# Kernel tuning notes

Measured on AMD Instinct MI355X. Metric: run time of the kernel, lower is better.

Reference implementation:

```python
import jax, jax.numpy as jnp
from jax import lax
import numpy as np

EPS = 1e-7  # keras.backend.epsilon()
DISCOUNT = 1.0

B, T, S, F = 32, 128, 64, 256  # samples, sentences, steps, features


def setup_inputs() -> dict:
    key = jax.random.key(0)
    ks = jax.random.split(key, 6)
    scale = 1.0 / np.sqrt(F)
    return {
        "x": jax.random.normal(ks[0], (B, T, S, F), dtype=jnp.float32),
        "W": jax.random.normal(ks[1], (F, F), dtype=jnp.float32) * scale,
        "W_context": jax.random.normal(ks[2], (F, F), dtype=jnp.float32) * scale,
        "W_l": jax.random.normal(ks[3], (F,), dtype=jnp.float32) * scale,
        "W_lc": jax.random.normal(ks[4], (F,), dtype=jnp.float32) * scale,
        "bl": jnp.zeros((1,), dtype=jnp.float32),
        "b": jnp.zeros((F,), dtype=jnp.float32),
        "u": jax.random.normal(ks[5], (F,), dtype=jnp.float32) * scale,
    }


def _forward(x, W, W_context, W_l, W_lc, bl, b, u):
    # x: [B, T, S, F]; scan over sentence axis T with carried context [B, F].
    def step(carry, x_):
        context, count = carry            # context: [B, F]
        context_ = context                # aggregate == 'sum'
        uit = jnp.einsum("bsf,fg->bsg", x_, W)            # [B, S, F]
        c = context_ @ W_context                            # [B, F]
        # gate: l = sigmoid(<context, W_lc> + bl broadcast over steps + <x, W_l>)
        gate_logit = (context_ @ W_lc + bl[0])[:, None] + x_ @ W_l  # [B, S]
        l = jax.nn.sigmoid(gate_logit)[..., None]           # [B, S, 1]
        uit = jnp.tanh(l * uit + (1.0 - l) * c[:, None, :] + b)
        ait = uit @ u                                        # [B, S]
        a = jnp.exp(ait)
        a = a / (jnp.sum(a, axis=1, keepdims=True) + EPS)   # masked-softmax (no mask)
        attended = jnp.einsum("bsf,bs->bf", x_, a)          # [B, F]
        new_context = context * DISCOUNT + attended
        return (new_context, count + 1.0), (attended, a, new_context)

    x_t = jnp.transpose(x, (1, 0, 2, 3))  # [T, B, S, F]
    init = (jnp.zeros((x.shape[0], x.shape[-1]), x.dtype), jnp.asarray(0.0, x.dtype))
    _, (out, weights, ctx) = lax.scan(step, init, x_t)
    output = jnp.transpose(out, (1, 0, 2))       # [B, T, F]
    context = jnp.transpose(ctx, (1, 0, 2))      # [B, T, F]
    weights = jnp.transpose(weights, (1, 0, 2))  # [B, T, S]
    return output, context, weights


def reference(x, W, W_context, W_l, W_lc, bl, b, u):
    return _forward(x, W, W_context, W_l, W_lc, bl, b, u)
```

## Files before the change

kernel.cpp:

```cpp
#include <hip/hip_runtime.h>
#include <stdint.h>

#define Tdim 128
#define Bdim 32
#define Sdim 64
#define Fdim 256

typedef unsigned short u16;
typedef short bf16x8 __attribute__((ext_vector_type(8)));
typedef float f32x4 __attribute__((ext_vector_type(4)));

#define K2     2.8853900817779268f
#define LOG2E  1.4426950408889634f

__device__ __forceinline__ u16 f2b(float f){
  union { float f; uint32_t u; } v; v.f = f;
  uint32_t u = v.u;
  if ((u & 0x7fffffffu) > 0x7f800000u) return (u16)0x7fc0;
  uint32_t r = (u + 0x7fffu + ((u >> 16) & 1u)) >> 16;
  return (u16)r;
}
__device__ __forceinline__ float b2f(u16 h){
  union { uint32_t u; float f; } v; v.u = ((uint32_t)h) << 16; return v.f;
}
__device__ __forceinline__ float b2f_lo(uint32_t w){
  union { uint32_t u; float f; } v; v.u = w << 16; return v.f;
}
__device__ __forceinline__ float b2f_hi(uint32_t w){
  union { uint32_t u; float f; } v; v.u = w & 0xffff0000u; return v.f;
}
__device__ __forceinline__ uint32_t pack2(float a, float b){
  return (uint32_t)f2b(a) | ((uint32_t)f2b(b) << 16);
}
__device__ __forceinline__ uint4 pack8(const float4 a, const float4 b){
  uint4 r;
  r.x = pack2(a.x, a.y); r.y = pack2(a.z, a.w);
  r.z = pack2(b.x, b.y); r.w = pack2(b.z, b.w);
  return r;
}

__device__ __forceinline__ void bar_lds(){
  asm volatile("s_waitcnt lgkmcnt(0)" ::: "memory");
  __builtin_amdgcn_s_barrier();
  asm volatile("" ::: "memory");
}


__global__ __launch_bounds__(256) void kt_transpose_cvt(const float* __restrict__ Wg,
                                                        u16* __restrict__ Wt){
  __shared__ u16 tile[64*66];
  int bx = blockIdx.x;
  int ti = bx >> 2, tj = bx & 3;
  int t = threadIdx.x;
#pragma unroll
  for (int i = 0; i < 16; ++i){
    int e = t*16 + i;
    int r = e >> 6, c = e & 63;
    tile[r*66 + c] = f2b(Wg[(ti*64 + r)*256 + tj*64 + c]);
  }
  __syncthreads();
#pragma unroll
  for (int i = 0; i < 16; ++i){
    int e = t*16 + i;
    int r = e >> 6, c = e & 63;
    Wt[(tj*64 + r)*256 + ti*64 + c] = tile[c*66 + r];
  }
}

__global__ __launch_bounds__(512, 4) void kt_gemm2(const float* __restrict__ Xg,
                                                   const u16* __restrict__ Wt,
                                                   const float* __restrict__ Wlg,
                                                   u16* __restrict__ Pg,
                                                   float* __restrict__ qg){
  __shared__ u16 Ws[256*72];
  __shared__ u16 Xs[128*72];
  __shared__ float Wls[256];
  int t  = threadIdx.x;
  int r0 = blockIdx.x * 128;
  if (t < 256) Wls[t] = Wlg[t];
  int lane = t & 63, wv = t >> 6;
  int goff = (wv & 3)*64, roff = (wv >> 2)*64;
  int fr = lane & 15, fq = lane >> 4;
  f32x4 acc[4][4];
#pragma unroll
  for (int a = 0; a < 4; ++a)
#pragma unroll
    for (int b = 0; b < 4; ++b)
      acc[a][b] = (f32x4){0.f,0.f,0.f,0.f};
  float qacc = 0.f;

  for (int kk = 0; kk < 4; ++kk){
    int k0 = kk*64;
    __syncthreads();
#pragma unroll
    for (int uu = 0; uu < 4; ++uu){
      int unit = uu*512 + t;
      int row = unit >> 3, c = unit & 7;
      *(uint4*)&Ws[row*72 + c*8] = *(const uint4*)&Wt[row*256 + k0 + c*8];
    }
#pragma unroll
    for (int uu = 0; uu < 2; ++uu){
      int unit = uu*512 + t;
      int row = unit >> 3, c = unit & 7;
      const float4* xp = (const float4*)&Xg[(size_t)(r0+row)*256 + k0 + c*8];
      *(uint4*)&Xs[row*72 + c*8] = pack8(xp[0], xp[1]);
    }
    __syncthreads();
    if (t < 128){
      int r = t;
#pragma unroll
      for (int c = 0; c < 8; ++c){
        uint4 xv = *(const uint4*)&Xs[r*72 + c*8];
        const uint32_t* xw = (const uint32_t*)&xv;
#pragma unroll
        for (int p = 0; p < 4; ++p){
          qacc = fmaf(b2f_lo(xw[p]), Wls[k0 + c*8 + 2*p],     qacc);
          qacc = fmaf(b2f_hi(xw[p]), Wls[k0 + c*8 + 2*p + 1], qacc);
        }
      }
    }
#pragma unroll
    for (int ks = 0; ks < 64; ks += 32){
      bf16x8 af[4], bf_[4];
#pragma unroll
      for (int mi = 0; mi < 4; ++mi)
        af[mi] = *(const bf16x8*)&Ws[(goff + mi*16 + fr)*72 + ks + fq*8];
#pragma unroll
      for (int ni = 0; ni < 4; ++ni)
        bf_[ni] = *(const bf16x8*)&Xs[(roff + ni*16 + fr)*72 + ks + fq*8];
#pragma unroll
      for (int mi = 0; mi < 4; ++mi)
#pragma unroll
        for (int ni = 0; ni < 4; ++ni)
          acc[mi][ni] = __builtin_amdgcn_mfma_f32_16x16x32_bf16(
              af[mi], bf_[ni], acc[mi][ni], 0, 0, 0);
    }
  }
#pragma unroll
  for (int mi = 0; mi < 4; ++mi){
    int g = goff + mi*16 + fq*4;
    int grp = g >> 4;
#pragma unroll
    for (int ni = 0; ni < 4; ++ni){
      int r = r0 + roff + ni*16 + fr;
      int bt = r >> 6, s = r & 63;
      ushort4 st;
      st.x = f2b(acc[mi][ni][0]); st.y = f2b(acc[mi][ni][1]);
      st.z = f2b(acc[mi][ni][2]); st.w = f2b(acc[mi][ni][3]);
      *(ushort4*)&Pg[(size_t)bt*16384 + grp*1024 + s*16 + fq*4] = st;
    }
  }
  if (t < 128) qg[r0 + t] = qacc;
}

__global__ __launch_bounds__(1024, 4) void kt_scan6(
    const float* __restrict__ Xg, const u16* __restrict__ Pf,
    const float* __restrict__ qf, const float* __restrict__ Wcg,
    const float* __restrict__ Wlcg, const float* __restrict__ blg,
    const float* __restrict__ biasg, const float* __restrict__ ug,
    float* __restrict__ out)
{
  __shared__ float ctx_s[256], bbr_s[256], ur_s[256], wlc_s[256];
  __shared__ float pp[64*17];
  __shared__ float attp[16*260];
  __shared__ float glc_p[4];

  const int tid   = threadIdx.x;
  const int b     = blockIdx.x;
  const int lane  = tid & 63;
  const int wave  = tid >> 6;
  const int g_loc = lane >> 2;
  const int fc    = lane & 3;
  const int gcol  = wave*16 + g_loc;
  const int f     = tid & 255;

  uint32_t wcp2[32];
#pragma unroll
  for (int i = 0; i < 16; ++i){
    int m  = (4*fc + i) & 15;
    int fb = fc*64 + m*4;
    wcp2[2*i]   = pack2(Wcg[(fb+0)*256 + gcol], Wcg[(fb+1)*256 + gcol]);
    wcp2[2*i+1] = pack2(Wcg[(fb+2)*256 + gcol], Wcg[(fb+3)*256 + gcol]);
  }

  if (tid < 256){
    ctx_s[tid] = 0.f;
    bbr_s[tid] = K2 * biasg[tid];
    ur_s[tid]  = ug[tid];
    wlc_s[tid] = Wlcg[tid];
  }
  if (tid < 4) glc_p[tid] = 0.f;
  const float blf = blg[0];
  float glcr = 0.f;

  const u16*    pP = Pf + (size_t)(b*Tdim)*16384 + wave*1024 + lane*16;
  const float4* pX = (const float4*)Xg + (size_t)(b*Tdim)*4096 + wave*256 + lane;
  const float*  pq = qf + (size_t)(b*Tdim)*64 + lane;

  uint32_t pw[8];
  {
    const uint4* pp_ = (const uint4*)pP;
    *(uint4*)&pw[0] = pp_[0]; *(uint4*)&pw[4] = pp_[1];
  }
  float qcur = pq[0];

  float* outO = out;
  float* outC = out + Bdim*Tdim*Fdim;
  float* outW = out + 2*Bdim*Tdim*Fdim;
  __syncthreads();

  for (int tt = 0; tt < Tdim; ++tt){
    const int bt    = b*Tdim + tt;
    const int nstep = (tt < Tdim-1) ? 1 : 0;

    uint32_t pwn[8];
    {
      const uint4* pp_ = (const uint4*)(pP + (size_t)nstep*16384);
      *(uint4*)&pwn[0] = pp_[0]; *(uint4*)&pwn[4] = pp_[1];
    }
    float qn = pq[nstep*64];
    float4 x0 = pX[0], x1 = pX[64], x2 = pX[128], x3 = pX[192];

    {
      glcr += glc_p[0] + glc_p[1] + glc_p[2] + glc_p[3];
      float logit = glcr + blf + qcur;
      float sig = __builtin_amdgcn_rcpf(1.f + __builtin_exp2f(-LOG2E*logit));
      const float l2  = K2 * sig;
      const float l2b = K2 - K2*sig;

      float pa = 0.f;
#pragma unroll
      for (int i = 0; i < 16; ++i){
        int m = (4*fc + i) & 15;
        float4 cv = *(const float4*)&ctx_s[fc*64 + m*4];
        pa = fmaf(cv.x, b2f_lo(wcp2[2*i]),   pa);
        pa = fmaf(cv.y, b2f_hi(wcp2[2*i]),   pa);
        pa = fmaf(cv.z, b2f_lo(wcp2[2*i+1]), pa);
        pa = fmaf(cv.w, b2f_hi(wcp2[2*i+1]), pa);
      }
      pa += __shfl_xor(pa, 1, 64);
      pa += __shfl_xor(pa, 2, 64);
      float c[16];
#pragma unroll
      for (int j = 0; j < 16; ++j)
        c[j] = __shfl(pa, 4*j, 64);

      float ait = 0.f;
#pragma unroll
      for (int j = 0; j < 16; ++j){
        float pv = (j & 1) ? b2f_hi(pw[j>>1]) : b2f_lo(pw[j>>1]);
        float bb = bbr_s[wave*16 + j];
        float uu = ur_s[wave*16 + j];
        float z  = fmaf(l2, pv, fmaf(l2b, c[j], bb));
        float e  = __builtin_exp2f(z);
        float r  = __builtin_amdgcn_rcpf(e + 1.f);
        ait += fmaf(-2.f*uu, r, uu);
      }
      pp[lane*17 + wave] = ait;
    }
    bar_lds();

    {
      const int ppb = lane*17;
      float ait = 0.f;
#pragma unroll
      for (int k = 0; k < 16; ++k) ait += pp[ppb + k];
      float mx = ait;
#pragma unroll
      for (int off = 32; off > 0; off >>= 1)
        mx = fmaxf(mx, __shfl_xor(mx, off, 64));
      float e = __builtin_exp2f(LOG2E*(ait - mx));
      float ssum = e;
#pragma unroll
      for (int off = 32; off > 0; off >>= 1)
        ssum += __shfl_xor(ssum, off, 64);
      float denom = ssum + 1e-7f * __builtin_exp2f(-LOG2E*mx);
      float a = e * __builtin_amdgcn_rcpf(denom);
      if (wave == 0) outW[(size_t)bt*Sdim + lane] = a;

      const float av0 = __shfl(a, wave*4 + 0, 64);
      const float av1 = __shfl(a, wave*4 + 1, 64);
      const float av2 = __shfl(a, wave*4 + 2, 64);
      const float av3 = __shfl(a, wave*4 + 3, 64);
      float4 acc;
      acc.x = av0*x0.x; acc.y = av0*x0.y; acc.z = av0*x0.z; acc.w = av0*x0.w;
      acc.x = fmaf(av1, x1.x, acc.x); acc.y = fmaf(av1, x1.y, acc.y);
      acc.z = fmaf(av1, x1.z, acc.z); acc.w = fmaf(av1, x1.w, acc.w);
      acc.x = fmaf(av2, x2.x, acc.x); acc.y = fmaf(av2, x2.y, acc.y);
      acc.z = fmaf(av2, x2.z, acc.z); acc.w = fmaf(av2, x2.w, acc.w);
      acc.x = fmaf(av3, x3.x, acc.x); acc.y = fmaf(av3, x3.y, acc.y);
      acc.z = fmaf(av3, x3.z, acc.z); acc.w = fmaf(av3, x3.w, acc.w);
      *(float4*)&attp[wave*260 + lane*4] = acc;
    }
    bar_lds();

    if (tid < 256){
      float att = 0.f;
#pragma unroll
      for (int k = 0; k < 16; ++k) att += attp[k*260 + f];
      const size_t o = (size_t)bt*Fdim + f;
      outO[o] = att;
      float nc = ctx_s[f] + att;
      ctx_s[f] = nc;
      outC[o] = nc;
      float gp = att * wlc_s[f];
#pragma unroll
      for (int off = 32; off > 0; off >>= 1)
        gp += __shfl_xor(gp, off, 64);
      if (lane == 0) glc_p[wave] = gp;
    }
    bar_lds();

#pragma unroll
    for (int k = 0; k < 8; ++k) pw[k] = pwn[k];
    qcur = qn;
    pP += (size_t)nstep*16384;
    pX += 4096;
    pq += 64;
  }
}

__global__ __launch_bounds__(1024) void fused_ctx_attn(
    const float* __restrict__ Xg, const float* __restrict__ Wg,
    const float* __restrict__ Wcg, const float* __restrict__ Wlg,
    const float* __restrict__ Wlcg, const float* __restrict__ blg,
    const float* __restrict__ biasg, const float* __restrict__ ug,
    float* __restrict__ out)
{
  __shared__ u16   xs[64*272];
  __shared__ float ps[64*257];
  __shared__ float cpart[8*258];
  __shared__ float qp[64*5];
  __shared__ float pp[64*17];
  __shared__ float attp[4*260];
  __shared__ float ctx_s[256], c_s[256], bb_s[256], u_s[256], wlc_s[256], wl_s[256];
  __shared__ float l2_s[64], l2b_s[64], a_s[64];
  __shared__ float glc_p[4];

  const int tid  = threadIdx.x;
  const int b    = blockIdx.x;
  const int lane = tid & 63;
  const int wave = tid >> 6;
  const int fr   = lane & 15;
  const int fq   = lane >> 4;
  const int f    = tid & 255;
  const int sb   = tid >> 8;

  bf16x8 afW[8];
  {
    const int gcol = wave*16 + fr;
#pragma unroll
    for (int kt = 0; kt < 8; ++kt){
      u16 tmp[8];
#pragma unroll
      for (int j = 0; j < 8; ++j)
        tmp[j] = f2b(Wg[(kt*32 + fq*8 + j)*256 + gcol]);
      afW[kt] = *(const bf16x8*)tmp;
    }
  }
  const int fj = tid >> 7;
  const int gp = tid & 127;
  uint32_t wcp[32];
#pragma unroll
  for (int fi = 0; fi < 32; ++fi)
    wcp[fi] = pack2(Wcg[(fj*32 + fi)*256 + gp*2], Wcg[(fj*32 + fi)*256 + gp*2 + 1]);

  if (tid < 256){
    ctx_s[tid] = 0.f;
    bb_s[tid]  = K2 * biasg[tid];
    u_s[tid]   = ug[tid];
    wlc_s[tid] = Wlcg[tid];
    wl_s[tid]  = Wlg[tid];
  }
  if (tid < 4) glc_p[tid] = 0.f;
  const float blf = blg[0];
  float glcr = 0.f;

  float* outO = out;
  float* outC = out + Bdim*Tdim*Fdim;
  float* outW = out + 2*Bdim*Tdim*Fdim;

  const int srow = tid >> 5;
  const int sc8  = (tid & 31)*8;
  {
    const long xb = (long)(b*Tdim)*Sdim*Fdim;
    const float4* p0 = (const float4*)&Xg[xb + (long)srow*256 + sc8];
    const float4* p1 = (const float4*)&Xg[xb + (long)(srow+32)*256 + sc8];
    *(uint4*)&xs[srow*272 + sc8]      = pack8(p0[0], p0[1]);
    *(uint4*)&xs[(srow+32)*272 + sc8] = pack8(p1[0], p1[1]);
  }
  __syncthreads();

  for (int tt = 0; tt < Tdim; ++tt){
    const int tn = (tt < Tdim-1) ? (tt+1) : tt;
    const long xb = (long)((b*Tdim + tn))*Sdim*Fdim;
    const float4* p0 = (const float4*)&Xg[xb + (long)srow*256 + sc8];
    const float4* p1 = (const float4*)&Xg[xb + (long)(srow+32)*256 + sc8];
    uint4 xr0 = pack8(p0[0], p0[1]);
    uint4 xr1 = pack8(p1[0], p1[1]);

    {
      float pa = 0.f, pb = 0.f;
#pragma unroll
      for (int fi = 0; fi < 32; ++fi){
        float cf = ctx_s[fj*32 + fi];
        pa = fmaf(cf, b2f_lo(wcp[fi]), pa);
        pb = fmaf(cf, b2f_hi(wcp[fi]), pb);
      }
      float2 st; st.x = pa; st.y = pb;
      *(float2*)&cpart[fj*258 + gp*2] = st;
    }
    {
      f32x4 acc[4];
#pragma unroll
      for (int nt = 0; nt < 4; ++nt) acc[nt] = (f32x4){0.f,0.f,0.f,0.f};
#pragma unroll
      for (int kt = 0; kt < 8; ++kt){
#pragma unroll
        for (int nt = 0; nt < 4; ++nt){
          bf16x8 bfx = *(const bf16x8*)&xs[(nt*16 + fr)*272 + kt*32 + fq*8];
          acc[nt] = __builtin_amdgcn_mfma_f32_16x16x32_bf16(afW[kt], bfx, acc[nt], 0, 0, 0);
        }
      }
#pragma unroll
      for (int nt = 0; nt < 4; ++nt){
        const int s = nt*16 + fr;
        const int g = wave*16 + fq*4;
        ps[s*257 + g + 0] = acc[nt][0];
        ps[s*257 + g + 1] = acc[nt][1];
        ps[s*257 + g + 2] = acc[nt][2];
        ps[s*257 + g + 3] = acc[nt][3];
      }
    }
    if (tid < 256){
      const int s = tid >> 2, qtr = tid & 3;
      float a = 0.f;
#pragma unroll
      for (int j = 0; j < 64; ++j)
        a = fmaf(b2f(xs[s*272 + qtr*64 + j]), wl_s[qtr*64 + j], a);
      qp[s*5 + qtr] = a;
    }
    __syncthreads();

    if (tid < 256){
      float a = 0.f;
#pragma unroll
      for (int k = 0; k < 8; ++k) a += cpart[k*258 + tid];
      c_s[tid] = a;
    }
    if (tid < 64){
      glcr += glc_p[0] + glc_p[1] + glc_p[2] + glc_p[3];
      float q = qp[tid*5] + qp[tid*5+1] + qp[tid*5+2] + qp[tid*5+3];
      float logit = glcr + blf + q;
      float sig = 1.f / (1.f + __builtin_exp2f(-LOG2E*logit));
      l2_s[tid]  = K2 * sig;
      l2b_s[tid] = K2 - K2*sig;
    }
    __syncthreads();

    {
      const float cf = c_s[f], bbf = bb_s[f], uf = u_s[f], n2 = -2.f*u_s[f];
#pragma unroll
      for (int i = 0; i < 16; ++i){
        const int s = sb*16 + i;
        float z2 = fmaf(l2_s[s], ps[s*257 + f], fmaf(l2b_s[s], cf, bbf));
        float e  = __builtin_exp2f(z2);
        float r  = 1.f / (e + 1.f);
        ps[s*257 + f] = fmaf(n2, r, uf);
      }
    }
    __syncthreads();

    {
      const int s = tid & 63, grp = tid >> 6;
      float a = 0.f;
#pragma unroll
      for (int k = 0; k < 16; ++k) a += ps[s*257 + grp*16 + k];
      pp[s*17 + grp] = a;
    }
    __syncthreads();

    if (tid < 64){
      const int s = tid;
      float ait = 0.f;
#pragma unroll
      for (int k = 0; k < 16; ++k) ait += pp[s*17 + k];
      float m = ait;
#pragma unroll
      for (int off = 32; off > 0; off >>= 1)
        m = fmaxf(m, __shfl_xor(m, off, 64));
      float e = __builtin_exp2f(LOG2E*(ait - m));
      float ssum = e;
#pragma unroll
      for (int off = 32; off > 0; off >>= 1)
        ssum += __shfl_xor(ssum, off, 64);
      float denom = ssum + 1e-7f * __builtin_exp2f(-LOG2E*m);
      float a = e / denom;
      a_s[s] = a;
      outW[(b*Tdim + tt)*Sdim + s] = a;
    }
    __syncthreads();

    {
      float ap = 0.f;
#pragma unroll
      for (int i = 0; i < 16; ++i){
        const int s = sb*16 + i;
        ap = fmaf(a_s[s], b2f(xs[s*272 + f]), ap);
      }
      attp[sb*260 + f] = ap;
    }
    __syncthreads();

    if (tid < 256){
      float att = attp[f] + attp[260+f] + attp[520+f] + attp[780+f];
      const int o = (b*Tdim + tt)*Fdim + f;
      outO[o] = att;
      float nc = ctx_s[f] + att;
      ctx_s[f] = nc;
      outC[o] = nc;
      float gpart = att * wlc_s[f];
#pragma unroll
      for (int off = 32; off > 0; off >>= 1)
        gpart += __shfl_xor(gpart, off, 64);
      if (lane == 0) glc_p[wave] = gpart;
    }
    *(uint4*)&xs[srow*272 + sc8] = xr0;
    *(uint4*)&xs[(srow+32)*272 + sc8] = xr1;
    __syncthreads();
  }
}

extern "C" void kernel_launch(void* const* d_in, const int* in_sizes, int n_in,
                              void* d_out, int out_size, void* d_ws, size_t ws_size,
                              hipStream_t stream){
  const float* x    = (const float*)d_in[0];
  const float* W    = (const float*)d_in[1];
  const float* Wc   = (const float*)d_in[2];
  const float* Wl   = (const float*)d_in[3];
  const float* Wlc  = (const float*)d_in[4];
  const float* bl   = (const float*)d_in[5];
  const float* bias = (const float*)d_in[6];
  const float* u    = (const float*)d_in[7];
  float* out = (float*)d_out;

  const size_t P_BYTES  = (size_t)4096*16384*2;
  const size_t Q_BYTES  = (size_t)262144*4;
  const size_t WT_BYTES = (size_t)256*256*2;
  const size_t NEED = P_BYTES + Q_BYTES + WT_BYTES;

  if (ws_size >= NEED){
    uint8_t* ws = (uint8_t*)d_ws;
    u16*   P  = (u16*)ws;
    float* q  = (float*)(ws + P_BYTES);
    u16*   Wt = (u16*)(ws + P_BYTES + Q_BYTES);
    kt_transpose_cvt<<<16, 256, 0, stream>>>(W, Wt);
    kt_gemm2<<<2048, 512, 0, stream>>>(x, Wt, Wl, P, q);
    kt_scan6<<<Bdim, 1024, 0, stream>>>(x, P, q, Wc, Wlc, bl, bias, u, out);
  } else {
    fused_ctx_attn<<<Bdim, 1024, 0, stream>>>(x, W, Wc, Wl, Wlc, bl, bias, u, out);
  }
}
```

Baseline: 1.082 ms.

## Merge GEMM producer and scan consumer into one flag-synchronized kernel

Replaces the separate projection-GEMM launch and scan launch with one kernel. The first 32 blocks run the sequential per-batch scan, and the remaining blocks compute projection chunks in time order, publishing per-chunk flags with release stores. Consumers spin on acquire loads before using each chunk, so the GEMM overlaps the latency-bound scan instead of running before it. The softmax max-subtraction is also removed, which saves two shuffle reductions per step but risks overflow for large attention logits. The scheme also depends on consumer blocks being resident, or it can deadlock.

```diff
diff --git a/kernel.cpp b/kernel.cpp
--- a/kernel.cpp
+++ b/kernel.cpp
@@ -5,6 +5,8 @@
 #define Bdim 32
 #define Sdim 64
 #define Fdim 256
+#define NCONS 32
+#define NPROD 1024
 
 typedef unsigned short u16;
 typedef short bf16x8 __attribute__((ext_vector_type(8)));
@@ -47,11 +49,14 @@
 
 
 __global__ __launch_bounds__(256) void kt_transpose_cvt(const float* __restrict__ Wg,
-                                                        u16* __restrict__ Wt){
+                                                        u16* __restrict__ Wt,
+                                                        int* __restrict__ flags){
   __shared__ u16 tile[64*66];
   int bx = blockIdx.x;
   int ti = bx >> 2, tj = bx & 3;
   int t = threadIdx.x;
+  int gid = bx*256 + t;
+  if (gid < NCONS*64) flags[gid] = 0;
 #pragma unroll
   for (int i = 0; i < 16; ++i){
     int e = t*16 + i;
@@ -67,105 +72,124 @@
   }
 }
 
-__global__ __launch_bounds__(512, 4) void kt_gemm2(const float* __restrict__ Xg,
-                                                   const u16* __restrict__ Wt,
-                                                   const float* __restrict__ Wlg,
-                                                   u16* __restrict__ Pg,
-                                                   float* __restrict__ qg){
-  __shared__ u16 Ws[256*72];
-  __shared__ u16 Xs[128*72];
-  __shared__ float Wls[256];
-  int t  = threadIdx.x;
-  int r0 = blockIdx.x * 128;
-  if (t < 256) Wls[t] = Wlg[t];
-  int lane = t & 63, wv = t >> 6;
-  int goff = (wv & 3)*64, roff = (wv >> 2)*64;
-  int fr = lane & 15, fq = lane >> 4;
-  f32x4 acc[4][4];
-#pragma unroll
-  for (int a = 0; a < 4; ++a)
-#pragma unroll
-    for (int b = 0; b < 4; ++b)
-      acc[a][b] = (f32x4){0.f,0.f,0.f,0.f};
-  float qacc = 0.f;
-
-  for (int kk = 0; kk < 4; ++kk){
-    int k0 = kk*64;
-    __syncthreads();
-#pragma unroll
-    for (int uu = 0; uu < 4; ++uu){
-      int unit = uu*512 + t;
-      int row = unit >> 3, c = unit & 7;
-      *(uint4*)&Ws[row*72 + c*8] = *(const uint4*)&Wt[row*256 + k0 + c*8];
-    }
-#pragma unroll
-    for (int uu = 0; uu < 2; ++uu){
-      int unit = uu*512 + t;
-      int row = unit >> 3, c = unit & 7;
-      const float4* xp = (const float4*)&Xg[(size_t)(r0+row)*256 + k0 + c*8];
-      *(uint4*)&Xs[row*72 + c*8] = pack8(xp[0], xp[1]);
-    }
-    __syncthreads();
-    if (t < 128){
-      int r = t;
-#pragma unroll
-      for (int c = 0; c < 8; ++c){
-        uint4 xv = *(const uint4*)&Xs[r*72 + c*8];
-        const uint32_t* xw = (const uint32_t*)&xv;
-#pragma unroll
-        for (int p = 0; p < 4; ++p){
-          qacc = fmaf(b2f_lo(xw[p]), Wls[k0 + c*8 + 2*p],     qacc);
-          qacc = fmaf(b2f_hi(xw[p]), Wls[k0 + c*8 + 2*p + 1], qacc);
-        }
-      }
-    }
-#pragma unroll
-    for (int ks = 0; ks < 64; ks += 32){
-      bf16x8 af[4], bf_[4];
-#pragma unroll
-      for (int mi = 0; mi < 4; ++mi)
-        af[mi] = *(const bf16x8*)&Ws[(goff + mi*16 + fr)*72 + ks + fq*8];
-#pragma unroll
-      for (int ni = 0; ni < 4; ++ni)
-        bf_[ni] = *(const bf16x8*)&Xs[(roff + ni*16 + fr)*72 + ks + fq*8];
-#pragma unroll
-      for (int mi = 0; mi < 4; ++mi)
-#pragma unroll
-        for (int ni = 0; ni < 4; ++ni)
-          acc[mi][ni] = __builtin_amdgcn_mfma_f32_16x16x32_bf16(
-              af[mi], bf_[ni], acc[mi][ni], 0, 0, 0);
-    }
-  }
-#pragma unroll
-  for (int mi = 0; mi < 4; ++mi){
-    int g = goff + mi*16 + fq*4;
-    int grp = g >> 4;
-#pragma unroll
-    for (int ni = 0; ni < 4; ++ni){
-      int r = r0 + roff + ni*16 + fr;
-      int bt = r >> 6, s = r & 63;
-      ushort4 st;
-      st.x = f2b(acc[mi][ni][0]); st.y = f2b(acc[mi][ni][1]);
-      st.z = f2b(acc[mi][ni][2]); st.w = f2b(acc[mi][ni][3]);
-      *(ushort4*)&Pg[(size_t)bt*16384 + grp*1024 + s*16 + fq*4] = st;
-    }
-  }
-  if (t < 128) qg[r0 + t] = qacc;
-}
-
-__global__ __launch_bounds__(1024, 4) void kt_scan6(
-    const float* __restrict__ Xg, const u16* __restrict__ Pf,
-    const float* __restrict__ qf, const float* __restrict__ Wcg,
+__global__ __launch_bounds__(1024, 4) void kt_combined(
+    const float* __restrict__ Xg, const u16* __restrict__ Wt,
+    const float* __restrict__ Wlg, const float* __restrict__ Wcg,
     const float* __restrict__ Wlcg, const float* __restrict__ blg,
     const float* __restrict__ biasg, const float* __restrict__ ug,
-    float* __restrict__ out)
+    u16* __restrict__ Pg, float* __restrict__ qg,
+    int* __restrict__ flags, float* __restrict__ out)
 {
-  __shared__ float ctx_s[256], bbr_s[256], ur_s[256], wlc_s[256];
-  __shared__ float pp[64*17];
-  __shared__ float attp[16*260];
-  __shared__ float glc_p[4];
-
-  const int tid   = threadIdx.x;
+  __shared__ union ShMem {
+    struct {
+      u16 Ws[2][256*72];
+      u16 Xs[2][128*72];
+      float Wls[256];
+    } p;
+    struct {
+      float ctx[256], bbr[256], ur[256], wlc[256];
+      float pp[64*17];
+      float attp[16*260];
+      float glc[4];
+    } c;
+  } sh;
+
+  const int tid = threadIdx.x;
+
+  if (blockIdx.x >= NCONS){
+    const int p   = blockIdx.x - NCONS;
+    const int h   = tid >> 9;
+    const int t   = tid & 511;
+    const int hg  = p*2 + h;
+    const int bb  = hg & 31;
+    const int tq2 = hg >> 5;
+    const int r0  = bb*8192 + tq2*128;
+    u16* __restrict__ Ws = sh.p.Ws[h];
+    u16* __restrict__ Xs = sh.p.Xs[h];
+    float* Wls = sh.p.Wls;
+    if (tid < 256) Wls[tid] = Wlg[tid];
+    const int lane = t & 63, wv = t >> 6;
+    const int goff = (wv & 3)*64, roff = (wv >> 2)*64;
+    const int fr = lane & 15, fq = lane >> 4;
+    f32x4 acc[4][4];
+#pragma unroll
+    for (int a = 0; a < 4; ++a)
+#pragma unroll
+      for (int b2 = 0; b2 < 4; ++b2)
+        acc[a][b2] = (f32x4){0.f,0.f,0.f,0.f};
+    float qacc = 0.f;
+
+    for (int kk = 0; kk < 4; ++kk){
+      int k0 = kk*64;
+      __syncthreads();
+#pragma unroll
+      for (int uu = 0; uu < 4; ++uu){
+        int unit = uu*512 + t;
+        int row = unit >> 3, cc = unit & 7;
+        *(uint4*)&Ws[row*72 + cc*8] = *(const uint4*)&Wt[row*256 + k0 + cc*8];
+      }
+#pragma unroll
+      for (int uu = 0; uu < 2; ++uu){
+        int unit = uu*512 + t;
+        int row = unit >> 3, cc = unit & 7;
+        const float4* xp = (const float4*)&Xg[(size_t)(r0+row)*256 + k0 + cc*8];
+        *(uint4*)&Xs[row*72 + cc*8] = pack8(xp[0], xp[1]);
+      }
+      __syncthreads();
+      if (t < 128){
+        int r = t;
+#pragma unroll
+        for (int cc = 0; cc < 8; ++cc){
+          uint4 xv = *(const uint4*)&Xs[r*72 + cc*8];
+          const uint32_t* xw = (const uint32_t*)&xv;
+#pragma unroll
+          for (int q2 = 0; q2 < 4; ++q2){
+            qacc = fmaf(b2f_lo(xw[q2]), Wls[k0 + cc*8 + 2*q2],     qacc);
+            qacc = fmaf(b2f_hi(xw[q2]), Wls[k0 + cc*8 + 2*q2 + 1], qacc);
+          }
+        }
+      }
+#pragma unroll
+      for (int ks = 0; ks < 64; ks += 32){
+        bf16x8 af[4], bf_[4];
+#pragma unroll
+        for (int mi = 0; mi < 4; ++mi)
+          af[mi] = *(const bf16x8*)&Ws[(goff + mi*16 + fr)*72 + ks + fq*8];
+#pragma unroll
+        for (int ni = 0; ni < 4; ++ni)
+          bf_[ni] = *(const bf16x8*)&Xs[(roff + ni*16 + fr)*72 + ks + fq*8];
+#pragma unroll
+        for (int mi = 0; mi < 4; ++mi)
+#pragma unroll
+          for (int ni = 0; ni < 4; ++ni)
+            acc[mi][ni] = __builtin_amdgcn_mfma_f32_16x16x32_bf16(
+                af[mi], bf_[ni], acc[mi][ni], 0, 0, 0);
+      }
+    }
+#pragma unroll
+    for (int mi = 0; mi < 4; ++mi){
+      int g = goff + mi*16 + fq*4;
+      int grp = g >> 4;
+#pragma unroll
+      for (int ni = 0; ni < 4; ++ni){
+        int r = r0 + roff + ni*16 + fr;
+        int bt = r >> 6, s = r & 63;
+        ushort4 st;
+        st.x = f2b(acc[mi][ni][0]); st.y = f2b(acc[mi][ni][1]);
+        st.z = f2b(acc[mi][ni][2]); st.w = f2b(acc[mi][ni][3]);
+        *(ushort4*)&Pg[(size_t)bt*16384 + grp*1024 + s*16 + fq*4] = st;
+      }
+    }
+    if (t < 128) qg[r0 + t] = qacc;
+    __syncthreads();
+    if (t == 0){
+      __threadfence();
+      __hip_atomic_store(&flags[bb*64 + tq2], 1,
+                         __ATOMIC_RELEASE, __HIP_MEMORY_SCOPE_AGENT);
+    }
+    return;
+  }
+
   const int b     = blockIdx.x;
   const int lane  = tid & 63;
   const int wave  = tid >> 6;
@@ -184,18 +208,25 @@
   }
 
   if (tid < 256){
-    ctx_s[tid] = 0.f;
-    bbr_s[tid] = K2 * biasg[tid];
-    ur_s[tid]  = ug[tid];
-    wlc_s[tid] = Wlcg[tid];
-  }
-  if (tid < 4) glc_p[tid] = 0.f;
+    sh.c.ctx[tid] = 0.f;
+    sh.c.bbr[tid] = K2 * biasg[tid];
+    sh.c.ur[tid]  = ug[tid];
+    sh.c.wlc[tid] = Wlcg[tid];
+  }
+  if (tid < 4) sh.c.glc[tid] = 0.f;
   const float blf = blg[0];
   float glcr = 0.f;
 
-  const u16*    pP = Pf + (size_t)(b*Tdim)*16384 + wave*1024 + lane*16;
+  if (tid == 0){
+    while (__hip_atomic_load(&flags[b*64], __ATOMIC_ACQUIRE,
+                             __HIP_MEMORY_SCOPE_AGENT) == 0)
+      __builtin_amdgcn_s_sleep(4);
+  }
+  __syncthreads();
+
+  const u16*    pP = Pg + (size_t)(b*Tdim)*16384 + wave*1024 + lane*16;
   const float4* pX = (const float4*)Xg + (size_t)(b*Tdim)*4096 + wave*256 + lane;
-  const float*  pq = qf + (size_t)(b*Tdim)*64 + lane;
+  const float*  pq = qg + (size_t)(b*Tdim)*64 + lane;
 
   uint32_t pw[8];
   {
@@ -207,7 +238,6 @@
   float* outO = out;
   float* outC = out + Bdim*Tdim*Fdim;
   float* outW = out + 2*Bdim*Tdim*Fdim;
-  __syncthreads();
 
   for (int tt = 0; tt < Tdim; ++tt){
     const int bt    = b*Tdim + tt;
@@ -222,7 +252,7 @@
     float4 x0 = pX[0], x1 = pX[64], x2 = pX[128], x3 = pX[192];
 
     {
-      glcr += glc_p[0] + glc_p[1] + glc_p[2] + glc_p[3];
+      glcr += sh.c.glc[0] + sh.c.glc[1] + sh.c.glc[2] + sh.c.glc[3];
       float logit = glcr + blf + qcur;
       float sig = __builtin_amdgcn_rcpf(1.f + __builtin_exp2f(-LOG2E*logit));
       const float l2  = K2 * sig;
@@ -232,7 +262,7 @@
 #pragma unroll
       for (int i = 0; i < 16; ++i){
         int m = (4*fc + i) & 15;
-        float4 cv = *(const float4*)&ctx_s[fc*64 + m*4];
+        float4 cv = *(const float4*)&sh.c.ctx[fc*64 + m*4];
         pa = fmaf(cv.x, b2f_lo(wcp2[2*i]),   pa);
         pa = fmaf(cv.y, b2f_hi(wcp2[2*i]),   pa);
         pa = fmaf(cv.z, b2f_lo(wcp2[2*i+1]), pa);
@@ -249,14 +279,14 @@
 #pragma unroll
       for (int j = 0; j < 16; ++j){
         float pv = (j & 1) ? b2f_hi(pw[j>>1]) : b2f_lo(pw[j>>1]);
-        float bb = bbr_s[wave*16 + j];
-        float uu = ur_s[wave*16 + j];
+        float bb = sh.c.bbr[wave*16 + j];
+        float uu = sh.c.ur[wave*16 + j];
         float z  = fmaf(l2, pv, fmaf(l2b, c[j], bb));
         float e  = __builtin_exp2f(z);
         float r  = __builtin_amdgcn_rcpf(e + 1.f);
         ait += fmaf(-2.f*uu, r, uu);
       }
-      pp[lane*17 + wave] = ait;
+      sh.c.pp[lane*17 + wave] = ait;
     }
     bar_lds();
 
@@ -264,18 +294,13 @@
       const int ppb = lane*17;
       float ait = 0.f;
 #pragma unroll
-      for (int k = 0; k < 16; ++k) ait += pp[ppb + k];
-      float mx = ait;
-#pragma unroll
-      for (int off = 32; off > 0; off >>= 1)
-        mx = fmaxf(mx, __shfl_xor(mx, off, 64));
-      float e = __builtin_exp2f(LOG2E*(ait - mx));
+      for (int k = 0; k < 16; ++k) ait += sh.c.pp[ppb + k];
+      float e = __builtin_exp2f(LOG2E*ait);
       float ssum = e;
 #pragma unroll
       for (int off = 32; off > 0; off >>= 1)
         ssum += __shfl_xor(ssum, off, 64);
-      float denom = ssum + 1e-7f * __builtin_exp2f(-LOG2E*mx);
-      float a = e * __builtin_amdgcn_rcpf(denom);
+      float a = e * __builtin_amdgcn_rcpf(ssum + 1e-7f);
       if (wave == 0) outW[(size_t)bt*Sdim + lane] = a;
 
       const float av0 = __shfl(a, wave*4 + 0, 64);
@@ -290,24 +315,30 @@
       acc.z = fmaf(av2, x2.z, acc.z); acc.w = fmaf(av2, x2.w, acc.w);
       acc.x = fmaf(av3, x3.x, acc.x); acc.y = fmaf(av3, x3.y, acc.y);
       acc.z = fmaf(av3, x3.z, acc.z); acc.w = fmaf(av3, x3.w, acc.w);
-      *(float4*)&attp[wave*260 + lane*4] = acc;
+      *(float4*)&sh.c.attp[wave*260 + lane*4] = acc;
     }
     bar_lds();
 
     if (tid < 256){
       float att = 0.f;
 #pragma unroll
-      for (int k = 0; k < 16; ++k) att += attp[k*260 + f];
+      for (int k = 0; k < 16; ++k) att += sh.c.attp[k*260 + f];
       const size_t o = (size_t)bt*Fdim + f;
       outO[o] = att;
-      float nc = ctx_s[f] + att;
-      ctx_s[f] = nc;
+      float nc = sh.c.ctx[f] + att;
+      sh.c.ctx[f] = nc;
       outC[o] = nc;
-      float gp = att * wlc_s[f];
+      float gp = att * sh.c.wlc[f];
 #pragma unroll
       for (int off = 32; off > 0; off >>= 1)
         gp += __shfl_xor(gp, off, 64);
-      if (lane == 0) glc_p[wave] = gp;
+      if (lane == 0) sh.c.glc[wave] = gp;
+    }
+    if (tid == 0 && (tt & 1) == 0 && tt <= Tdim-4){
+      const int g = (tt + 2) >> 1;
+      while (__hip_atomic_load(&flags[b*64 + g], __ATOMIC_ACQUIRE,
+                               __HIP_MEMORY_SCOPE_AGENT) == 0)
+        __builtin_amdgcn_s_sleep(4);
     }
     bar_lds();
 
@@ -547,16 +578,18 @@
   const size_t P_BYTES  = (size_t)4096*16384*2;
   const size_t Q_BYTES  = (size_t)262144*4;
   const size_t WT_BYTES = (size_t)256*256*2;
-  const size_t NEED = P_BYTES + Q_BYTES + WT_BYTES;
+  const size_t FL_BYTES = (size_t)2048*4;
+  const size_t NEED = P_BYTES + Q_BYTES + WT_BYTES + FL_BYTES;
 
   if (ws_size >= NEED){
     uint8_t* ws = (uint8_t*)d_ws;
-    u16*   P  = (u16*)ws;
-    float* q  = (float*)(ws + P_BYTES);
-    u16*   Wt = (u16*)(ws + P_BYTES + Q_BYTES);
-    kt_transpose_cvt<<<16, 256, 0, stream>>>(W, Wt);
-    kt_gemm2<<<2048, 512, 0, stream>>>(x, Wt, Wl, P, q);
-    kt_scan6<<<Bdim, 1024, 0, stream>>>(x, P, q, Wc, Wlc, bl, bias, u, out);
+    u16*   P     = (u16*)ws;
+    float* q     = (float*)(ws + P_BYTES);
+    u16*   Wt    = (u16*)(ws + P_BYTES + Q_BYTES);
+    int*   flags = (int*)(ws + P_BYTES + Q_BYTES + WT_BYTES);
+    kt_transpose_cvt<<<16, 256, 0, stream>>>(W, Wt, flags);
+    kt_combined<<<NCONS + NPROD, 1024, 0, stream>>>(
+        x, Wt, Wl, Wc, Wlc, bl, bias, u, P, q, flags, out);
   } else {
     fused_ctx_attn<<<Bdim, 1024, 0, stream>>>(x, W, Wc, Wl, Wlc, bl, bias, u, out);
   }
```

Result: slower. 1.246 ms (+15.1%).
